# Kernel optimization log

Measured on AMD Instinct MI355X. Metric: run time of the kernel, lower is better.

The kernel has to match this reference:

```python
import jax, jax.numpy as jnp
import numpy as np

B, IN, H, NB = 8192, 1024, 2048, 8
BS = H // NB  # 256


def setup_inputs() -> dict:
    key = jax.random.key(0)
    ks = jax.random.split(key, 4)
    s = 0.02
    return {
        "x": jax.random.normal(ks[0], (B, IN), dtype=jnp.float32),
        "h": jax.random.normal(ks[1], (B, H), dtype=jnp.float32),
        "W_ir": jax.random.normal(ks[2], (3 * H, IN), dtype=jnp.float32) * s,
        "b_ir_lin": jnp.zeros((3 * H,), dtype=jnp.float32),
        "b_ir": jnp.zeros((3 * H,), dtype=jnp.float32),
        "W_h": jax.random.normal(ks[3], (NB, 3 * BS, BS), dtype=jnp.float32) * s,
        "b_hr": jnp.zeros((3 * H,), dtype=jnp.float32),
    }


def reference(x, h, W_ir, b_ir_lin, b_ir, W_h, b_hr):
    b = x.shape[0]
    nb, three_bs, bs = W_h.shape
    hdim = nb * bs
    # input projection: w_ir(x) + b_ir  -> [B, 3H], chunked globally into r,z,n
    wx = x @ W_ir.T + b_ir_lin + b_ir
    wxr, wxz, wxn = jnp.split(wx, 3, axis=1)
    wxr = wxr.reshape(b, nb, bs)
    wxz = wxz.reshape(b, nb, bs)
    wxn = wxn.reshape(b, nb, bs)
    # block-diagonal hidden projection: per-block Linear(bs -> 3*bs), no bias
    hb = h.reshape(b, nb, bs)
    # b_hr is sliced in contiguous chunks of 3*bs per block (local r,z,n layout)
    wh = jnp.einsum('bki,koi->bko', hb, W_h) + b_hr.reshape(nb, three_bs)
    whr, whz, whn = jnp.split(wh, 3, axis=2)
    r = jax.nn.sigmoid(wxr + whr)
    z = jax.nn.sigmoid(wxz + whz)
    n = jnp.tanh(wxn + r * whn)
    h_new = (1.0 - z) * hb + z * n
    return h_new.reshape(b, hdim)
```

## Files before the change

### kernel.cpp

```cpp
#include <hip/hip_runtime.h>
#include <cstdint>
#include <cstddef>


typedef __attribute__((ext_vector_type(8))) short bf16x8;
typedef __attribute__((ext_vector_type(4))) float f32x4;

__device__ __forceinline__ unsigned short f2bf(float f) {
    uint32_t u = __float_as_uint(f);
    u += 0x7FFFu + ((u >> 16) & 1u);
    return (unsigned short)(u >> 16);
}

__device__ __forceinline__ void gload16(const void* g, void* l) {
    __builtin_amdgcn_global_load_lds(
        (const __attribute__((address_space(1))) void*)g,
        (__attribute__((address_space(3))) void*)l,
        16, 0, 0);
}

__device__ __forceinline__ float sigmoidf_(float x) {
    return 1.0f / (1.0f + __expf(-x));
}
__device__ __forceinline__ float tanhf_(float x) {
    float e = __expf(-2.0f * fabsf(x));
    float t = (1.0f - e) / (1.0f + e);
    return copysignf(t, x);
}

__global__ __launch_bounds__(256)
void cast_f32_to_bf16(const float* __restrict__ s, unsigned short* __restrict__ d, int n4) {
    int i = blockIdx.x * 256 + threadIdx.x;
    if (i >= n4) return;
    const float4 v = *reinterpret_cast<const float4*>(s + (size_t)i * 4);
    ushort4 o;
    o.x = f2bf(v.x); o.y = f2bf(v.y); o.z = f2bf(v.z); o.w = f2bf(v.w);
    *reinterpret_cast<ushort4*>(d + (size_t)i * 4) = o;
}


#define MFMA12(n_, NT) do {                                                    \
    asm volatile("s_waitcnt lgkmcnt(0)" ::: "memory");                         \
    __builtin_amdgcn_sched_barrier(0);                                         \
    __builtin_amdgcn_s_setprio(1);                                             \
    _Pragma("unroll")                                                          \
    for (int m_ = 0; m_ < 4; ++m_) {                                           \
        acc[0][m_][n_] = __builtin_amdgcn_mfma_f32_16x16x32_bf16(              \
            av[m_], bv[0], acc[0][m_][n_], 0, 0, 0);                           \
        acc[1][m_][n_] = __builtin_amdgcn_mfma_f32_16x16x32_bf16(              \
            av[m_], bv[1], acc[1][m_][n_], 0, 0, 0);                           \
        acc[NT][m_][n_] = __builtin_amdgcn_mfma_f32_16x16x32_bf16(             \
            av[m_], bv[2], acc[NT][m_][n_], 0, 0, 0);                          \
    }                                                                          \
    __builtin_amdgcn_s_setprio(0);                                             \
} while (0)

#define LDA(m, kb_) (*(const bf16x8*)(aS + (wm * 64 + (m) * 16 + fr) * 64 + (kb_)))
#define LDB(s, n_, kb_) (*(const bf16x8*)(bS + ((s) * 64 + wn * 32 + (n_) * 16 + fr) * 64 + (kb_)))

#define I0_1(kt, ds) do {                                                      \
    gload16(b1[0] + (size_t)(kt) * 64, Bs + (ds) * 12288 + 0 * 2048 + doff);   \
    gload16(b1[1] + (size_t)(kt) * 64, Bs + (ds) * 12288 + 1 * 2048 + doff);   \
    gload16(b1[2] + (size_t)(kt) * 64, Bs + (ds) * 12288 + 2 * 2048 + doff);   \
    gload16(b1[3] + (size_t)(kt) * 64, Bs + (ds) * 12288 + 3 * 2048 + doff); } while (0)
#define I1_1(kt, ds) do {                                                      \
    gload16(b1[4] + (size_t)(kt) * 64, Bs + (ds) * 12288 + 4 * 2048 + doff);   \
    gload16(b1[5] + (size_t)(kt) * 64, Bs + (ds) * 12288 + 5 * 2048 + doff);   \
    gload16(a1[0] + (size_t)(kt) * 64, As + (ds) * 8192 + 0 * 2048 + doff);    \
    gload16(a1[1] + (size_t)(kt) * 64, As + (ds) * 8192 + 1 * 2048 + doff); } while (0)
#define I2_1(kt, ds) do {                                                      \
    gload16(a1[2] + (size_t)(kt) * 64, As + (ds) * 8192 + 2 * 2048 + doff);    \
    gload16(a1[3] + (size_t)(kt) * 64, As + (ds) * 8192 + 3 * 2048 + doff); } while (0)
#define I0_2(k2, ds) do {                                                      \
    gload16(b2[0] + (size_t)(k2) * 64, Bs + (ds) * 12288 + 0 * 2048 + doff);   \
    gload16(b2[1] + (size_t)(k2) * 64, Bs + (ds) * 12288 + 1 * 2048 + doff);   \
    gload16(b2[2] + (size_t)(k2) * 64, Bs + (ds) * 12288 + 2 * 2048 + doff);   \
    gload16(b2[3] + (size_t)(k2) * 64, Bs + (ds) * 12288 + 3 * 2048 + doff); } while (0)
#define I1_2(k2, ds) do {                                                      \
    gload16(b2[4] + (size_t)(k2) * 64, Bs + (ds) * 12288 + 4 * 2048 + doff);   \
    gload16(b2[5] + (size_t)(k2) * 64, Bs + (ds) * 12288 + 5 * 2048 + doff);   \
    gload16(a2[0] + (size_t)(k2) * 64, As + (ds) * 8192 + 0 * 2048 + doff);    \
    gload16(a2[1] + (size_t)(k2) * 64, As + (ds) * 8192 + 1 * 2048 + doff); } while (0)
#define I2_2(k2, ds) do {                                                      \
    gload16(a2[2] + (size_t)(k2) * 64, As + (ds) * 8192 + 2 * 2048 + doff);    \
    gload16(a2[3] + (size_t)(k2) * 64, As + (ds) * 8192 + 3 * 2048 + doff); } while (0)

#define KSTEP(slot_, I0, W0, I1, I2, NT) do {                                  \
    const unsigned short* aS = As + (slot_) * 8192;                            \
    const unsigned short* bS = Bs + (slot_) * 12288;                           \
    I0;                                                                        \
    asm volatile("s_waitcnt vmcnt(" W0 ")" ::: "memory");                      \
    __builtin_amdgcn_s_barrier();                                              \
    _Pragma("unroll") for (int m_ = 0; m_ < 4; ++m_) av[m_] = LDA(m_, kb0);    \
    _Pragma("unroll") for (int s_ = 0; s_ < 3; ++s_) bv[s_] = LDB(s_, 0, kb0); \
    MFMA12(0, NT);                                                             \
    I1;                                                                        \
    _Pragma("unroll") for (int s_ = 0; s_ < 3; ++s_) bv[s_] = LDB(s_, 1, kb0); \
    MFMA12(1, NT);                                                             \
    I2;                                                                        \
    _Pragma("unroll") for (int m_ = 0; m_ < 4; ++m_) av[m_] = LDA(m_, kb1);    \
    _Pragma("unroll") for (int s_ = 0; s_ < 3; ++s_) bv[s_] = LDB(s_, 0, kb1); \
    MFMA12(0, NT);                                                             \
    _Pragma("unroll") for (int s_ = 0; s_ < 3; ++s_) bv[s_] = LDB(s_, 1, kb1); \
    MFMA12(1, NT);                                                             \
    __builtin_amdgcn_s_barrier();                                              \
} while (0)

__global__ __launch_bounds__(256, 2)
void gru_fused(const unsigned short* __restrict__ Xb,
               const unsigned short* __restrict__ Wirb,
               const unsigned short* __restrict__ Hbb,
               const unsigned short* __restrict__ Whb,
               const float* __restrict__ b_ir_lin,
               const float* __restrict__ b_ir,
               const float* __restrict__ b_hr,
               const float* __restrict__ Hf,
               float* __restrict__ out) {
    constexpr int K1 = 1024, H = 2048;
    __shared__ unsigned short lds[2 * 8192 + 2 * 12288];
    unsigned short* const As = lds;
    unsigned short* const Bs = lds + 2 * 8192;

    const int tid  = threadIdx.x;
    const int lane = tid & 63;
    const int w    = tid >> 6;
    const int wm   = w >> 1;
    const int wn   = w & 1;

    const int bid  = blockIdx.x;
    const int kb   = bid & 7;
    const int idx  = bid >> 3;
    const int bm   = (idx >> 2) * 128;
    const int hsub = idx & 3;
    const int hcb  = kb * 256 + hsub * 64;

    const int srow  = tid >> 3;
    const int chunk = (tid & 7) ^ (srow & 7);
    const int scol  = chunk * 8;
    const int doff  = tid * 8;
    const unsigned short* a1[4];
    const unsigned short* a2[4];
    #pragma unroll
    for (int q = 0; q < 4; ++q) {
        a1[q] = Xb  + (size_t)(bm + q * 32 + srow) * K1 + scol;
        a2[q] = Hbb + (size_t)(bm + q * 32 + srow) * H + kb * 256 + scol;
    }
    const unsigned short* b1[6];
    const unsigned short* b2[6];
    #pragma unroll
    for (int q = 0; q < 6; ++q) {
        const int s  = q >> 1;
        const int rr = (q & 1) * 32 + srow;
        b1[q] = Wirb + (size_t)(s * 2048 + hcb + rr) * K1 + scol;
        b2[q] = Whb + (size_t)kb * 196608 + (size_t)(s * 256 + hsub * 64 + rr) * 256 + scol;
    }

    const int fr  = lane & 15;
    const int k0e = (lane >> 4) * 8;
    const int mfr = (fr & 7) << 4;
    const int kb0 = ((k0e * 2) ^ mfr) >> 1;
    const int kb1 = (((k0e * 2) + 64) ^ mfr) >> 1;

    f32x4 acc[4][4][2] = {};
    bf16x8 av[4], bv[3];

    I0_1(0, 0); I1_1(0, 0); I2_1(0, 0);

    #pragma unroll 1
    for (int t = 0; t < 15; ++t) {
        const int sl = t & 1, nx = sl ^ 1;
        KSTEP(sl, I0_1(t + 1, nx), "4", I1_1(t + 1, nx), I2_1(t + 1, nx), 2);
    }
    KSTEP(1, I0_2(0, 0), "4", I1_2(0, 0), I2_2(0, 0), 2);
    #pragma unroll 1
    for (int t = 16; t < 19; ++t) {
        const int sl = t & 1, nx = sl ^ 1;
        KSTEP(sl, I0_2(t - 15, nx), "4", I1_2(t - 15, nx), I2_2(t - 15, nx), 3);
    }
    KSTEP(1, ((void)0), "0", ((void)0), ((void)0), 3);

    const int rq = (lane >> 4) * 4;
    #pragma unroll
    for (int n = 0; n < 2; ++n) {
        const int hcol = hcb + wn * 32 + n * 16 + fr;
        const int lcol = hcol & 255;
        const float bir0 = b_ir_lin[hcol]        + b_ir[hcol];
        const float bir1 = b_ir_lin[2048 + hcol] + b_ir[2048 + hcol];
        const float bir2 = b_ir_lin[4096 + hcol] + b_ir[4096 + hcol];
        const float bhr0 = b_hr[kb * 768 + lcol];
        const float bhr1 = b_hr[kb * 768 + 256 + lcol];
        const float bhr2 = b_hr[kb * 768 + 512 + lcol];
        #pragma unroll
        for (int mi = 0; mi < 4; ++mi) {
            #pragma unroll
            for (int r = 0; r < 4; ++r) {
                const int row = bm + wm * 64 + mi * 16 + rq + r;
                const float pr = acc[0][mi][n][r] + bir0 + bhr0;
                const float pz = acc[1][mi][n][r] + bir1 + bhr1;
                const float xn = acc[2][mi][n][r] + bir2;
                const float hn = acc[3][mi][n][r] + bhr2;
                const float rg = sigmoidf_(pr);
                const float zg = sigmoidf_(pz);
                const float ng = tanhf_(xn + rg * hn);
                const float hv = Hf[(size_t)row * H + hcol];
                out[(size_t)row * H + hcol] = (1.0f - zg) * hv + zg * ng;
            }
        }
    }
}

extern "C" void kernel_launch(void* const* d_in, const int* in_sizes, int n_in,
                              void* d_out, int out_size, void* d_ws, size_t ws_size,
                              hipStream_t stream) {
    const float* x        = (const float*)d_in[0];
    const float* h        = (const float*)d_in[1];
    const float* W_ir     = (const float*)d_in[2];
    const float* b_ir_lin = (const float*)d_in[3];
    const float* b_ir     = (const float*)d_in[4];
    const float* W_h      = (const float*)d_in[5];
    const float* b_hr     = (const float*)d_in[6];
    float* out = (float*)d_out;

    char* ws = (char*)d_ws;
    unsigned short* xb   = (unsigned short*)(ws);
    unsigned short* wirb = (unsigned short*)(ws + 16777216);
    unsigned short* hb   = (unsigned short*)(ws + 29360128);
    unsigned short* whb  = (unsigned short*)(ws + 62914560);

    cast_f32_to_bf16<<<8192,  256, 0, stream>>>(x,    xb,   2097152);
    cast_f32_to_bf16<<<6144,  256, 0, stream>>>(W_ir, wirb, 1572864);
    cast_f32_to_bf16<<<16384, 256, 0, stream>>>(h,    hb,   4194304);
    cast_f32_to_bf16<<<1536,  256, 0, stream>>>(W_h,  whb,  393216);

    gru_fused<<<2048, 256, 0, stream>>>(xb, wirb, hb, whb,
                                        b_ir_lin, b_ir, b_hr, h, out);
}
```

Before: 177.6 us.

## Switch to 32x32x16 MFMA with new LDS layout, merge cast kernels, read bf16 h

```diff
diff --git a/kernel.cpp b/kernel.cpp
--- a/kernel.cpp
+++ b/kernel.cpp
@@ -4,12 +4,15 @@
 
 
 typedef __attribute__((ext_vector_type(8))) short bf16x8;
-typedef __attribute__((ext_vector_type(4))) float f32x4;
+typedef __attribute__((ext_vector_type(16))) float f32x16;
 
 __device__ __forceinline__ unsigned short f2bf(float f) {
     uint32_t u = __float_as_uint(f);
     u += 0x7FFFu + ((u >> 16) & 1u);
     return (unsigned short)(u >> 16);
+}
+__device__ __forceinline__ float bf2f(unsigned short b) {
+    return __uint_as_float(((uint32_t)b) << 16);
 }
 
 __device__ __forceinline__ void gload16(const void* g, void* l) {
@@ -29,61 +32,65 @@
 }
 
 __global__ __launch_bounds__(256)
-void cast_f32_to_bf16(const float* __restrict__ s, unsigned short* __restrict__ d, int n4) {
-    int i = blockIdx.x * 256 + threadIdx.x;
-    if (i >= n4) return;
-    const float4 v = *reinterpret_cast<const float4*>(s + (size_t)i * 4);
+void cast_all(const float* __restrict__ x, const float* __restrict__ wir,
+              const float* __restrict__ h, const float* __restrict__ wh,
+              unsigned short* __restrict__ xb, unsigned short* __restrict__ wirb,
+              unsigned short* __restrict__ hb, unsigned short* __restrict__ whb) {
+    const int i = blockIdx.x * 256 + threadIdx.x;
+    const float* s; unsigned short* d; int j;
+    if (i < 2097152)      { s = x;   d = xb;   j = i; }
+    else if (i < 3670016) { s = wir; d = wirb; j = i - 2097152; }
+    else if (i < 7864320) { s = h;   d = hb;   j = i - 3670016; }
+    else                  { s = wh;  d = whb;  j = i - 7864320; }
+    const float4 v = *reinterpret_cast<const float4*>(s + (size_t)j * 4);
     ushort4 o;
     o.x = f2bf(v.x); o.y = f2bf(v.y); o.z = f2bf(v.z); o.w = f2bf(v.w);
-    *reinterpret_cast<ushort4*>(d + (size_t)i * 4) = o;
-}
-
-
-#define MFMA12(n_, NT) do {                                                    \
-    asm volatile("s_waitcnt lgkmcnt(0)" ::: "memory");                         \
-    __builtin_amdgcn_sched_barrier(0);                                         \
-    __builtin_amdgcn_s_setprio(1);                                             \
-    _Pragma("unroll")                                                          \
-    for (int m_ = 0; m_ < 4; ++m_) {                                           \
-        acc[0][m_][n_] = __builtin_amdgcn_mfma_f32_16x16x32_bf16(              \
-            av[m_], bv[0], acc[0][m_][n_], 0, 0, 0);                           \
-        acc[1][m_][n_] = __builtin_amdgcn_mfma_f32_16x16x32_bf16(              \
-            av[m_], bv[1], acc[1][m_][n_], 0, 0, 0);                           \
-        acc[NT][m_][n_] = __builtin_amdgcn_mfma_f32_16x16x32_bf16(             \
-            av[m_], bv[2], acc[NT][m_][n_], 0, 0, 0);                          \
-    }                                                                          \
-    __builtin_amdgcn_s_setprio(0);                                             \
+    *reinterpret_cast<ushort4*>(d + (size_t)j * 4) = o;
+}
+
+
+#define IG(ptr, kt, dstbase) gload16((ptr) + (size_t)(kt) * 64, (dstbase) + doff)
+
+#define I0_1(kt, ds) do { IG(pB1[0], kt, Bs + (ds) * 12288 + 0 * 2048); \
+                          IG(pB1[1], kt, Bs + (ds) * 12288 + 1 * 2048); \
+                          IG(pB1[2], kt, Bs + (ds) * 12288 + 2 * 2048); \
+                          IG(pB1[3], kt, Bs + (ds) * 12288 + 3 * 2048); } while (0)
+#define I1_1(kt, ds) do { IG(pB1[4], kt, Bs + (ds) * 12288 + 4 * 2048); \
+                          IG(pB1[5], kt, Bs + (ds) * 12288 + 5 * 2048); \
+                          IG(pA1[0], kt, As + (ds) * 8192 + 0 * 2048);  \
+                          IG(pA1[1], kt, As + (ds) * 8192 + 1 * 2048); } while (0)
+#define I2_1(kt, ds) do { IG(pA1[2], kt, As + (ds) * 8192 + 2 * 2048);  \
+                          IG(pA1[3], kt, As + (ds) * 8192 + 3 * 2048); } while (0)
+#define I0_2(kt, ds) do { IG(pB2[0], kt, Bs + (ds) * 12288 + 0 * 2048); \
+                          IG(pB2[1], kt, Bs + (ds) * 12288 + 1 * 2048); \
+                          IG(pB2[2], kt, Bs + (ds) * 12288 + 2 * 2048); \
+                          IG(pB2[3], kt, Bs + (ds) * 12288 + 3 * 2048); } while (0)
+#define I1_2(kt, ds) do { IG(pB2[4], kt, Bs + (ds) * 12288 + 4 * 2048); \
+                          IG(pB2[5], kt, Bs + (ds) * 12288 + 5 * 2048); \
+                          IG(pA2[0], kt, As + (ds) * 8192 + 0 * 2048);  \
+                          IG(pA2[1], kt, As + (ds) * 8192 + 1 * 2048); } while (0)
+#define I2_2(kt, ds) do { IG(pA2[2], kt, As + (ds) * 8192 + 2 * 2048);  \
+                          IG(pA2[3], kt, As + (ds) * 8192 + 3 * 2048); } while (0)
+
+#define LDA32(mi, kk) (*(const bf16x8*)(aS + ((wm * 2 + (mi)) * 4 + (kk)) * 512 + l8))
+#define LDB32(s, kk)  (*(const bf16x8*)(bS + (((s) * 2 + wn) * 4 + (kk)) * 512 + l8))
+
+#define RDHALF(h_) do { \
+    av[0][0] = LDA32(0, 2 * (h_));     av[1][0] = LDA32(1, 2 * (h_));     \
+    bv[0][0] = LDB32(0, 2 * (h_));     bv[1][0] = LDB32(1, 2 * (h_));     \
+    bv[2][0] = LDB32(2, 2 * (h_));                                        \
+    av[0][1] = LDA32(0, 2 * (h_) + 1); av[1][1] = LDA32(1, 2 * (h_) + 1); \
+    bv[0][1] = LDB32(0, 2 * (h_) + 1); bv[1][1] = LDB32(1, 2 * (h_) + 1); \
+    bv[2][1] = LDB32(2, 2 * (h_) + 1); } while (0)
+
+#define FMA6(kl, NT) do { \
+    acc[0][0]  = __builtin_amdgcn_mfma_f32_32x32x16_bf16(av[0][kl], bv[0][kl], acc[0][0], 0, 0, 0);  \
+    acc[0][1]  = __builtin_amdgcn_mfma_f32_32x32x16_bf16(av[1][kl], bv[0][kl], acc[0][1], 0, 0, 0);  \
+    acc[1][0]  = __builtin_amdgcn_mfma_f32_32x32x16_bf16(av[0][kl], bv[1][kl], acc[1][0], 0, 0, 0);  \
+    acc[1][1]  = __builtin_amdgcn_mfma_f32_32x32x16_bf16(av[1][kl], bv[1][kl], acc[1][1], 0, 0, 0);  \
+    acc[NT][0] = __builtin_amdgcn_mfma_f32_32x32x16_bf16(av[0][kl], bv[2][kl], acc[NT][0], 0, 0, 0); \
+    acc[NT][1] = __builtin_amdgcn_mfma_f32_32x32x16_bf16(av[1][kl], bv[2][kl], acc[NT][1], 0, 0, 0); \
 } while (0)
-
-#define LDA(m, kb_) (*(const bf16x8*)(aS + (wm * 64 + (m) * 16 + fr) * 64 + (kb_)))
-#define LDB(s, n_, kb_) (*(const bf16x8*)(bS + ((s) * 64 + wn * 32 + (n_) * 16 + fr) * 64 + (kb_)))
-
-#define I0_1(kt, ds) do {                                                      \
-    gload16(b1[0] + (size_t)(kt) * 64, Bs + (ds) * 12288 + 0 * 2048 + doff);   \
-    gload16(b1[1] + (size_t)(kt) * 64, Bs + (ds) * 12288 + 1 * 2048 + doff);   \
-    gload16(b1[2] + (size_t)(kt) * 64, Bs + (ds) * 12288 + 2 * 2048 + doff);   \
-    gload16(b1[3] + (size_t)(kt) * 64, Bs + (ds) * 12288 + 3 * 2048 + doff); } while (0)
-#define I1_1(kt, ds) do {                                                      \
-    gload16(b1[4] + (size_t)(kt) * 64, Bs + (ds) * 12288 + 4 * 2048 + doff);   \
-    gload16(b1[5] + (size_t)(kt) * 64, Bs + (ds) * 12288 + 5 * 2048 + doff);   \
-    gload16(a1[0] + (size_t)(kt) * 64, As + (ds) * 8192 + 0 * 2048 + doff);    \
-    gload16(a1[1] + (size_t)(kt) * 64, As + (ds) * 8192 + 1 * 2048 + doff); } while (0)
-#define I2_1(kt, ds) do {                                                      \
-    gload16(a1[2] + (size_t)(kt) * 64, As + (ds) * 8192 + 2 * 2048 + doff);    \
-    gload16(a1[3] + (size_t)(kt) * 64, As + (ds) * 8192 + 3 * 2048 + doff); } while (0)
-#define I0_2(k2, ds) do {                                                      \
-    gload16(b2[0] + (size_t)(k2) * 64, Bs + (ds) * 12288 + 0 * 2048 + doff);   \
-    gload16(b2[1] + (size_t)(k2) * 64, Bs + (ds) * 12288 + 1 * 2048 + doff);   \
-    gload16(b2[2] + (size_t)(k2) * 64, Bs + (ds) * 12288 + 2 * 2048 + doff);   \
-    gload16(b2[3] + (size_t)(k2) * 64, Bs + (ds) * 12288 + 3 * 2048 + doff); } while (0)
-#define I1_2(k2, ds) do {                                                      \
-    gload16(b2[4] + (size_t)(k2) * 64, Bs + (ds) * 12288 + 4 * 2048 + doff);   \
-    gload16(b2[5] + (size_t)(k2) * 64, Bs + (ds) * 12288 + 5 * 2048 + doff);   \
-    gload16(a2[0] + (size_t)(k2) * 64, As + (ds) * 8192 + 0 * 2048 + doff);    \
-    gload16(a2[1] + (size_t)(k2) * 64, As + (ds) * 8192 + 1 * 2048 + doff); } while (0)
-#define I2_2(k2, ds) do {                                                      \
-    gload16(a2[2] + (size_t)(k2) * 64, As + (ds) * 8192 + 2 * 2048 + doff);    \
-    gload16(a2[3] + (size_t)(k2) * 64, As + (ds) * 8192 + 3 * 2048 + doff); } while (0)
 
 #define KSTEP(slot_, I0, W0, I1, I2, NT) do {                                  \
     const unsigned short* aS = As + (slot_) * 8192;                            \
@@ -91,18 +98,14 @@
     I0;                                                                        \
     asm volatile("s_waitcnt vmcnt(" W0 ")" ::: "memory");                      \
     __builtin_amdgcn_s_barrier();                                              \
-    _Pragma("unroll") for (int m_ = 0; m_ < 4; ++m_) av[m_] = LDA(m_, kb0);    \
-    _Pragma("unroll") for (int s_ = 0; s_ < 3; ++s_) bv[s_] = LDB(s_, 0, kb0); \
-    MFMA12(0, NT);                                                             \
+    RDHALF(0);                                                                 \
     I1;                                                                        \
-    _Pragma("unroll") for (int s_ = 0; s_ < 3; ++s_) bv[s_] = LDB(s_, 1, kb0); \
-    MFMA12(1, NT);                                                             \
+    __builtin_amdgcn_s_setprio(1); FMA6(0, NT); FMA6(1, NT);                   \
+    __builtin_amdgcn_s_setprio(0);                                             \
+    RDHALF(1);                                                                 \
     I2;                                                                        \
-    _Pragma("unroll") for (int m_ = 0; m_ < 4; ++m_) av[m_] = LDA(m_, kb1);    \
-    _Pragma("unroll") for (int s_ = 0; s_ < 3; ++s_) bv[s_] = LDB(s_, 0, kb1); \
-    MFMA12(0, NT);                                                             \
-    _Pragma("unroll") for (int s_ = 0; s_ < 3; ++s_) bv[s_] = LDB(s_, 1, kb1); \
-    MFMA12(1, NT);                                                             \
+    __builtin_amdgcn_s_setprio(1); FMA6(0, NT); FMA6(1, NT);                   \
+    __builtin_amdgcn_s_setprio(0);                                             \
     __builtin_amdgcn_s_barrier();                                              \
 } while (0)
 
@@ -114,7 +117,6 @@
                const float* __restrict__ b_ir_lin,
                const float* __restrict__ b_ir,
                const float* __restrict__ b_hr,
-               const float* __restrict__ Hf,
                float* __restrict__ out) {
     constexpr int K1 = 1024, H = 2048;
     __shared__ unsigned short lds[2 * 8192 + 2 * 12288];
@@ -126,6 +128,9 @@
     const int w    = tid >> 6;
     const int wm   = w >> 1;
     const int wn   = w & 1;
+    const int l31  = lane & 31;
+    const int lhi  = lane >> 5;
+    const int l8   = lane * 8;
 
     const int bid  = blockIdx.x;
     const int kb   = bid & 7;
@@ -134,35 +139,27 @@
     const int hsub = idx & 3;
     const int hcb  = kb * 256 + hsub * 64;
 
-    const int srow  = tid >> 3;
-    const int chunk = (tid & 7) ^ (srow & 7);
-    const int scol  = chunk * 8;
-    const int doff  = tid * 8;
-    const unsigned short* a1[4];
-    const unsigned short* a2[4];
+    const int kof  = w * 16 + lhi * 8;
+    const int doff = w * 512 + l8;
+    const unsigned short* pA1[4];
+    const unsigned short* pA2[4];
     #pragma unroll
-    for (int q = 0; q < 4; ++q) {
-        a1[q] = Xb  + (size_t)(bm + q * 32 + srow) * K1 + scol;
-        a2[q] = Hbb + (size_t)(bm + q * 32 + srow) * H + kb * 256 + scol;
-    }
-    const unsigned short* b1[6];
-    const unsigned short* b2[6];
+    for (int j = 0; j < 4; ++j) {
+        pA1[j] = Xb  + (size_t)(bm + j * 32 + l31) * K1 + kof;
+        pA2[j] = Hbb + (size_t)(bm + j * 32 + l31) * H + kb * 256 + kof;
+    }
+    const unsigned short* pB1[6];
+    const unsigned short* pB2[6];
     #pragma unroll
-    for (int q = 0; q < 6; ++q) {
-        const int s  = q >> 1;
-        const int rr = (q & 1) * 32 + srow;
-        b1[q] = Wirb + (size_t)(s * 2048 + hcb + rr) * K1 + scol;
-        b2[q] = Whb + (size_t)kb * 196608 + (size_t)(s * 256 + hsub * 64 + rr) * 256 + scol;
-    }
-
-    const int fr  = lane & 15;
-    const int k0e = (lane >> 4) * 8;
-    const int mfr = (fr & 7) << 4;
-    const int kb0 = ((k0e * 2) ^ mfr) >> 1;
-    const int kb1 = (((k0e * 2) + 64) ^ mfr) >> 1;
-
-    f32x4 acc[4][4][2] = {};
-    bf16x8 av[4], bv[3];
+    for (int g = 0; g < 6; ++g) {
+        const int s = g >> 1, hf = (g & 1) * 32;
+        pB1[g] = Wirb + (size_t)(s * 2048 + hcb + hf + l31) * K1 + kof;
+        pB2[g] = Whb + (size_t)kb * 196608
+                     + (size_t)(s * 256 + hsub * 64 + hf + l31) * 256 + kof;
+    }
+
+    f32x16 acc[4][2] = {};
+    bf16x8 av[2][2], bv[3][2];
 
     I0_1(0, 0); I1_1(0, 0); I2_1(0, 0);
 
@@ -179,32 +176,28 @@
     }
     KSTEP(1, ((void)0), "0", ((void)0), ((void)0), 3);
 
-    const int rq = (lane >> 4) * 4;
+    const int hcol = hcb + wn * 32 + l31;
+    const int lcol = hcol & 255;
+    const float bir0 = b_ir_lin[hcol]        + b_ir[hcol];
+    const float bir1 = b_ir_lin[2048 + hcol] + b_ir[2048 + hcol];
+    const float bir2 = b_ir_lin[4096 + hcol] + b_ir[4096 + hcol];
+    const float bhr0 = b_hr[kb * 768 + lcol];
+    const float bhr1 = b_hr[kb * 768 + 256 + lcol];
+    const float bhr2 = b_hr[kb * 768 + 512 + lcol];
     #pragma unroll
-    for (int n = 0; n < 2; ++n) {
-        const int hcol = hcb + wn * 32 + n * 16 + fr;
-        const int lcol = hcol & 255;
-        const float bir0 = b_ir_lin[hcol]        + b_ir[hcol];
-        const float bir1 = b_ir_lin[2048 + hcol] + b_ir[2048 + hcol];
-        const float bir2 = b_ir_lin[4096 + hcol] + b_ir[4096 + hcol];
-        const float bhr0 = b_hr[kb * 768 + lcol];
-        const float bhr1 = b_hr[kb * 768 + 256 + lcol];
-        const float bhr2 = b_hr[kb * 768 + 512 + lcol];
+    for (int mi = 0; mi < 2; ++mi) {
         #pragma unroll
-        for (int mi = 0; mi < 4; ++mi) {
-            #pragma unroll
-            for (int r = 0; r < 4; ++r) {
-                const int row = bm + wm * 64 + mi * 16 + rq + r;
-                const float pr = acc[0][mi][n][r] + bir0 + bhr0;
-                const float pz = acc[1][mi][n][r] + bir1 + bhr1;
-                const float xn = acc[2][mi][n][r] + bir2;
-                const float hn = acc[3][mi][n][r] + bhr2;
-                const float rg = sigmoidf_(pr);
-                const float zg = sigmoidf_(pz);
-                const float ng = tanhf_(xn + rg * hn);
-                const float hv = Hf[(size_t)row * H + hcol];
-                out[(size_t)row * H + hcol] = (1.0f - zg) * hv + zg * ng;
-            }
+        for (int r = 0; r < 16; ++r) {
+            const int row = bm + wm * 64 + mi * 32 + (r & 3) + 8 * (r >> 2) + 4 * lhi;
+            const float pr = acc[0][mi][r] + bir0 + bhr0;
+            const float pz = acc[1][mi][r] + bir1 + bhr1;
+            const float xn = acc[2][mi][r] + bir2;
+            const float hn = acc[3][mi][r] + bhr2;
+            const float rg = sigmoidf_(pr);
+            const float zg = sigmoidf_(pz);
+            const float ng = tanhf_(xn + rg * hn);
+            const float hv = bf2f(Hbb[(size_t)row * H + hcol]);
+            out[(size_t)row * H + hcol] = (1.0f - zg) * hv + zg * ng;
         }
     }
 }
@@ -227,11 +220,8 @@
     unsigned short* hb   = (unsigned short*)(ws + 29360128);
     unsigned short* whb  = (unsigned short*)(ws + 62914560);
 
-    cast_f32_to_bf16<<<8192,  256, 0, stream>>>(x,    xb,   2097152);
-    cast_f32_to_bf16<<<6144,  256, 0, stream>>>(W_ir, wirb, 1572864);
-    cast_f32_to_bf16<<<16384, 256, 0, stream>>>(h,    hb,   4194304);
-    cast_f32_to_bf16<<<1536,  256, 0, stream>>>(W_h,  whb,  393216);
+    cast_all<<<32256, 256, 0, stream>>>(x, W_ir, h, W_h, xb, wirb, hb, whb);
 
     gru_fused<<<2048, 256, 0, stream>>>(xb, wirb, hb, whb,
-                                        b_ir_lin, b_ir, b_hr, h, out);
-}
+                                        b_ir_lin, b_ir, b_hr, out);
+}
```

Result: slower. 231.1 us (+30.2%).

## Merge cast kernels, batch MFMA halves per k-step, read bf16 h in epilogue

Applied to the files above, without the earlier changes.

```diff
diff --git a/kernel.cpp b/kernel.cpp
--- a/kernel.cpp
+++ b/kernel.cpp
@@ -10,6 +10,9 @@
     uint32_t u = __float_as_uint(f);
     u += 0x7FFFu + ((u >> 16) & 1u);
     return (unsigned short)(u >> 16);
+}
+__device__ __forceinline__ float bf2f(unsigned short b) {
+    return __uint_as_float(((uint32_t)b) << 16);
 }
 
 __device__ __forceinline__ void gload16(const void* g, void* l) {
@@ -29,28 +32,41 @@
 }
 
 __global__ __launch_bounds__(256)
-void cast_f32_to_bf16(const float* __restrict__ s, unsigned short* __restrict__ d, int n4) {
-    int i = blockIdx.x * 256 + threadIdx.x;
-    if (i >= n4) return;
-    const float4 v = *reinterpret_cast<const float4*>(s + (size_t)i * 4);
+void cast_all(const float* __restrict__ x, const float* __restrict__ wir,
+              const float* __restrict__ h, const float* __restrict__ wh,
+              unsigned short* __restrict__ xb, unsigned short* __restrict__ wirb,
+              unsigned short* __restrict__ hb, unsigned short* __restrict__ whb) {
+    const int i = blockIdx.x * 256 + threadIdx.x;
+    const float* s; unsigned short* d; int j;
+    if (i < 2097152)      { s = x;   d = xb;   j = i; }
+    else if (i < 3670016) { s = wir; d = wirb; j = i - 2097152; }
+    else if (i < 7864320) { s = h;   d = hb;   j = i - 3670016; }
+    else                  { s = wh;  d = whb;  j = i - 7864320; }
+    const float4 v = *reinterpret_cast<const float4*>(s + (size_t)j * 4);
     ushort4 o;
     o.x = f2bf(v.x); o.y = f2bf(v.y); o.z = f2bf(v.z); o.w = f2bf(v.w);
-    *reinterpret_cast<ushort4*>(d + (size_t)i * 4) = o;
-}
-
-
-#define MFMA12(n_, NT) do {                                                    \
+    *reinterpret_cast<ushort4*>(d + (size_t)j * 4) = o;
+}
+
+
+#define MFMA24(NT) do {                                                        \
     asm volatile("s_waitcnt lgkmcnt(0)" ::: "memory");                         \
     __builtin_amdgcn_sched_barrier(0);                                         \
     __builtin_amdgcn_s_setprio(1);                                             \
     _Pragma("unroll")                                                          \
     for (int m_ = 0; m_ < 4; ++m_) {                                           \
-        acc[0][m_][n_] = __builtin_amdgcn_mfma_f32_16x16x32_bf16(              \
-            av[m_], bv[0], acc[0][m_][n_], 0, 0, 0);                           \
-        acc[1][m_][n_] = __builtin_amdgcn_mfma_f32_16x16x32_bf16(              \
-            av[m_], bv[1], acc[1][m_][n_], 0, 0, 0);                           \
-        acc[NT][m_][n_] = __builtin_amdgcn_mfma_f32_16x16x32_bf16(             \
-            av[m_], bv[2], acc[NT][m_][n_], 0, 0, 0);                          \
+        acc[0][m_][0] = __builtin_amdgcn_mfma_f32_16x16x32_bf16(               \
+            av[m_], bv[0][0], acc[0][m_][0], 0, 0, 0);                         \
+        acc[0][m_][1] = __builtin_amdgcn_mfma_f32_16x16x32_bf16(               \
+            av[m_], bv[0][1], acc[0][m_][1], 0, 0, 0);                         \
+        acc[1][m_][0] = __builtin_amdgcn_mfma_f32_16x16x32_bf16(               \
+            av[m_], bv[1][0], acc[1][m_][0], 0, 0, 0);                         \
+        acc[1][m_][1] = __builtin_amdgcn_mfma_f32_16x16x32_bf16(               \
+            av[m_], bv[1][1], acc[1][m_][1], 0, 0, 0);                         \
+        acc[NT][m_][0] = __builtin_amdgcn_mfma_f32_16x16x32_bf16(              \
+            av[m_], bv[2][0], acc[NT][m_][0], 0, 0, 0);                        \
+        acc[NT][m_][1] = __builtin_amdgcn_mfma_f32_16x16x32_bf16(              \
+            av[m_], bv[2][1], acc[NT][m_][1], 0, 0, 0);                        \
     }                                                                          \
     __builtin_amdgcn_s_setprio(0);                                             \
 } while (0)
@@ -92,17 +108,18 @@
     asm volatile("s_waitcnt vmcnt(" W0 ")" ::: "memory");                      \
     __builtin_amdgcn_s_barrier();                                              \
     _Pragma("unroll") for (int m_ = 0; m_ < 4; ++m_) av[m_] = LDA(m_, kb0);    \
-    _Pragma("unroll") for (int s_ = 0; s_ < 3; ++s_) bv[s_] = LDB(s_, 0, kb0); \
-    MFMA12(0, NT);                                                             \
+    _Pragma("unroll") for (int s_ = 0; s_ < 3; ++s_) {                         \
+        bv[s_][0] = LDB(s_, 0, kb0); bv[s_][1] = LDB(s_, 1, kb0); }            \
     I1;                                                                        \
-    _Pragma("unroll") for (int s_ = 0; s_ < 3; ++s_) bv[s_] = LDB(s_, 1, kb0); \
-    MFMA12(1, NT);                                                             \
+    __builtin_amdgcn_s_barrier();                                              \
+    MFMA24(NT);                                                                \
+    __builtin_amdgcn_s_barrier();                                              \
+    _Pragma("unroll") for (int m_ = 0; m_ < 4; ++m_) av[m_] = LDA(m_, kb1);    \
+    _Pragma("unroll") for (int s_ = 0; s_ < 3; ++s_) {                         \
+        bv[s_][0] = LDB(s_, 0, kb1); bv[s_][1] = LDB(s_, 1, kb1); }            \
     I2;                                                                        \
-    _Pragma("unroll") for (int m_ = 0; m_ < 4; ++m_) av[m_] = LDA(m_, kb1);    \
-    _Pragma("unroll") for (int s_ = 0; s_ < 3; ++s_) bv[s_] = LDB(s_, 0, kb1); \
-    MFMA12(0, NT);                                                             \
-    _Pragma("unroll") for (int s_ = 0; s_ < 3; ++s_) bv[s_] = LDB(s_, 1, kb1); \
-    MFMA12(1, NT);                                                             \
+    __builtin_amdgcn_s_barrier();                                              \
+    MFMA24(NT);                                                                \
     __builtin_amdgcn_s_barrier();                                              \
 } while (0)
 
@@ -114,7 +131,6 @@
                const float* __restrict__ b_ir_lin,
                const float* __restrict__ b_ir,
                const float* __restrict__ b_hr,
-               const float* __restrict__ Hf,
                float* __restrict__ out) {
     constexpr int K1 = 1024, H = 2048;
     __shared__ unsigned short lds[2 * 8192 + 2 * 12288];
@@ -162,7 +178,7 @@
     const int kb1 = (((k0e * 2) + 64) ^ mfr) >> 1;
 
     f32x4 acc[4][4][2] = {};
-    bf16x8 av[4], bv[3];
+    bf16x8 av[4], bv[3][2];
 
     I0_1(0, 0); I1_1(0, 0); I2_1(0, 0);
 
@@ -202,7 +218,7 @@
                 const float rg = sigmoidf_(pr);
                 const float zg = sigmoidf_(pz);
                 const float ng = tanhf_(xn + rg * hn);
-                const float hv = Hf[(size_t)row * H + hcol];
+                const float hv = bf2f(Hbb[(size_t)row * H + hcol]);
                 out[(size_t)row * H + hcol] = (1.0f - zg) * hv + zg * ng;
             }
         }
@@ -227,11 +243,8 @@
     unsigned short* hb   = (unsigned short*)(ws + 29360128);
     unsigned short* whb  = (unsigned short*)(ws + 62914560);
 
-    cast_f32_to_bf16<<<8192,  256, 0, stream>>>(x,    xb,   2097152);
-    cast_f32_to_bf16<<<6144,  256, 0, stream>>>(W_ir, wirb, 1572864);
-    cast_f32_to_bf16<<<16384, 256, 0, stream>>>(h,    hb,   4194304);
-    cast_f32_to_bf16<<<1536,  256, 0, stream>>>(W_h,  whb,  393216);
+    cast_all<<<32256, 256, 0, stream>>>(x, W_ir, h, W_h, xb, wirb, hb, whb);
 
     gru_fused<<<2048, 256, 0, stream>>>(xb, wirb, hb, whb,
-                                        b_ir_lin, b_ir, b_hr, h, out);
-}
+                                        b_ir_lin, b_ir, b_hr, out);
+}
```

New measurement: 170.6 us. 1.04x faster.
